# Performance work log

Measured on AMD Instinct MI355X. Metric: run time of the kernel, lower is better.

Reference implementation:

```python
import jax, jax.numpy as jnp
import numpy as np

EPS = 1e-5  # BatchNorm eps (torch default)

def setup_inputs() -> dict:
    key = jax.random.key(0)
    ks = jax.random.split(key, 24)
    B, NX, NY, F = 8, 128, 128, 128
    dims = [2 * F, 512, 256, 128, 64]
    d = {
        'x': jax.random.normal(ks[0], (B, NX, F), dtype=jnp.float32),
        'y': jax.random.normal(ks[1], (B, NY, F), dtype=jnp.float32),
    }
    i = 2
    for li, (din, dout) in enumerate(zip(dims[:-1], dims[1:]), start=1):
        d[f'w{li}'] = jax.random.normal(ks[i], (dout, din), dtype=jnp.float32) * (1.0 / np.sqrt(din)); i += 1
        d[f'b{li}'] = jax.random.normal(ks[i], (dout,), dtype=jnp.float32) * 0.02; i += 1
        if li < 4:  # BatchNorm1d on hidden layers only (eval mode: running stats)
            d[f'g{li}'] = 1.0 + 0.1 * jax.random.normal(ks[i], (dout,), dtype=jnp.float32); i += 1
            d[f'be{li}'] = 0.1 * jax.random.normal(ks[i], (dout,), dtype=jnp.float32); i += 1
            d[f'm{li}'] = 0.1 * jax.random.normal(ks[i], (dout,), dtype=jnp.float32); i += 1
            d[f'v{li}'] = 0.5 + jax.random.uniform(ks[i], (dout,), dtype=jnp.float32); i += 1
    return d

def _bn(h, g, be, m, v):
    # BatchNorm1d in eval mode over the channel (last) axis
    return (h - m) * (g * jax.lax.rsqrt(v + EPS)) + be

def reference(x, y,
              w1, b1, g1, be1, m1, v1,
              w2, b2, g2, be2, m2, v2,
              w3, b3, g3, be3, m3, v3,
              w4, b4):
    F = x.shape[-1]
    # First Linear on cat([x_i, y_j]) == split-weight broadcast add: avoids the
    # (B,nx,ny,2F) pairwise concat the torch code materializes (same math).
    wx, wy = w1[:, :F], w1[:, F:]                      # (512,F) each
    hx = jnp.einsum('bif,hf->bih', x, wx)              # (B,nx,512)
    hy = jnp.einsum('bjf,hf->bjh', y, wy)              # (B,ny,512)
    h = hx[:, :, None, :] + hy[:, None, :, :] + b1     # (B,nx,ny,512)
    h = jax.nn.relu(_bn(h, g1, be1, m1, v1))           # dropout is identity in eval
    h = jax.nn.relu(_bn(jnp.einsum('bijh,oh->bijo', h, w2) + b2, g2, be2, m2, v2))
    h = jax.nn.relu(_bn(jnp.einsum('bijh,oh->bijo', h, w3) + b3, g3, be3, m3, v3))
    e = jnp.einsum('bijh,oh->bijo', h, w4) + b4        # (B,nx,ny,64) embeddings
    # PSD path: einsum('bijk,bilk->bijl', e, e).sum(-1)
    #         == sum_k e[b,i,j,k] * (sum_l e[b,i,l,k])  -- avoids (B,nx,ny,ny)
    s = e.sum(axis=2)                                  # (B,nx,64)
    kernel = jnp.einsum('bijk,bik->bij', e, s)         # (B,nx,ny)
    return kernel
```

## Files before the change

### kernel.cpp

```cpp
#include <hip/hip_runtime.h>

#define EPS 1e-5f

typedef _Float16 half8 __attribute__((ext_vector_type(8)));
typedef _Float16 half4 __attribute__((ext_vector_type(4)));
typedef float f32x16 __attribute__((ext_vector_type(16)));
typedef float f32x4v __attribute__((ext_vector_type(4)));

__global__ __launch_bounds__(256)
void pre_kernel(
    const float* __restrict__ x, const float* __restrict__ y,
    const float* __restrict__ w1, const float* __restrict__ b1,
    const float* __restrict__ g1, const float* __restrict__ be1,
    const float* __restrict__ m1, const float* __restrict__ v1,
    const float* __restrict__ w2, const float* __restrict__ b2,
    const float* __restrict__ g2, const float* __restrict__ be2,
    const float* __restrict__ m2, const float* __restrict__ v2,
    const float* __restrict__ w3, const float* __restrict__ b3,
    const float* __restrict__ g3, const float* __restrict__ be3,
    const float* __restrict__ m3, const float* __restrict__ v3,
    const float* __restrict__ w4,
    _Float16* __restrict__ hxh, _Float16* __restrict__ hyh,
    _Float16* __restrict__ w2h, _Float16* __restrict__ w3h,
    _Float16* __restrict__ w4h,
    float* __restrict__ b2f, float* __restrict__ b3f)
{
    const int t = threadIdx.x;

    if (blockIdx.x >= 256) {
        int tid = (blockIdx.x - 256) * 256 + t;
        const int nth = 64 * 256;
        for (int idx = tid; idx < 256 * 512; idx += nth) {
            int n = idx >> 9;
            float a = g2[n] * rsqrtf(v2[n] + EPS);
            w2h[idx] = (_Float16)(a * w2[idx]);
        }
        for (int idx = tid; idx < 128 * 256; idx += nth) {
            int n = idx >> 8;
            float a = g3[n] * rsqrtf(v3[n] + EPS);
            w3h[idx] = (_Float16)(a * w3[idx]);
        }
        for (int idx = tid; idx < 64 * 128; idx += nth) {
            w4h[idx] = (_Float16)w4[idx];
        }
        if (tid < 256) {
            float a = g2[tid] * rsqrtf(v2[tid] + EPS);
            b2f[tid] = a * b2[tid] + be2[tid] - m2[tid] * a;
        } else if (tid < 384) {
            int n = tid - 256;
            float a = g3[n] * rsqrtf(v3[n] + EPS);
            b3f[n] = a * b3[n] + be3[n] - m3[n] * a;
        }
        return;
    }

    const int rg = blockIdx.x & 31;
    const int ng = (blockIdx.x >> 5) & 3;
    const int which = blockIdx.x >> 7;

    constexpr int LDA = 136;
    __shared__ _Float16 sh[32 * 136 + 128 * 136] __attribute__((aligned(16)));
    _Float16* xa = sh;
    _Float16* wb = sh + 32 * 136;

    const int rowbase = rg * 32;
    const float* src = which ? y : x;

#pragma unroll
    for (int p = 0; p < 4; ++p) {
        int c = p * 256 + t;
        int r = c >> 5, fo = (c & 31) * 4;
        f32x4v v = *(const f32x4v*)(src + (size_t)(rowbase + r) * 128 + fo);
        half4 h; h[0] = (_Float16)v[0]; h[1] = (_Float16)v[1];
        h[2] = (_Float16)v[2]; h[3] = (_Float16)v[3];
        *(half4*)(xa + r * LDA + fo) = h;
    }
#pragma unroll
    for (int p = 0; p < 16; ++p) {
        int c = p * 256 + t;
        int n = c >> 5, fo = (c & 31) * 4;
        f32x4v v = *(const f32x4v*)(w1 + (size_t)(ng * 128 + n) * 256 + which * 128 + fo);
        half4 h; h[0] = (_Float16)v[0]; h[1] = (_Float16)v[1];
        h[2] = (_Float16)v[2]; h[3] = (_Float16)v[3];
        *(half4*)(wb + n * LDA + fo) = h;
    }
    __syncthreads();

    const int wid = t >> 6;
    const int l = t & 63;
    const int l31 = l & 31, lh = l >> 5;

    f32x16 acc = (f32x16)0.f;
#pragma unroll
    for (int kc = 0; kc < 8; ++kc) {
        half8 af = *(const half8*)(xa + l31 * LDA + kc * 16 + lh * 8);
        half8 bf = *(const half8*)(wb + (wid * 32 + l31) * LDA + kc * 16 + lh * 8);
        acc = __builtin_amdgcn_mfma_f32_32x32x16_f16(af, bf, acc, 0, 0, 0);
    }

    const int n = ng * 128 + wid * 32 + l31;
    float alpha = g1[n] * rsqrtf(v1[n] + EPS);
    float bias = which ? 0.f : (alpha * b1[n] + be1[n] - m1[n] * alpha);
    _Float16* dst = which ? hyh : hxh;
#pragma unroll
    for (int r = 0; r < 16; ++r) {
        int m = (r & 3) + 8 * (r >> 2) + 4 * lh;
        dst[(size_t)(rowbase + m) * 512 + n] = (_Float16)(alpha * acc[r] + bias);
    }
}

__global__ __launch_bounds__(512, 4)
void fused_kernel(
    const _Float16* __restrict__ hxh, const _Float16* __restrict__ hyh,
    const _Float16* __restrict__ w2h, const _Float16* __restrict__ w3h,
    const _Float16* __restrict__ w4h,
    const float* __restrict__ b2f, const float* __restrict__ b3f,
    const float* __restrict__ b4,
    float* __restrict__ out)
{
    constexpr int LDK = 40;
    constexpr int LD2 = 264;
    constexpr int LD3 = 136;
    constexpr int LDE = 68;

    __shared__ char smem[3584 + 67584] __attribute__((aligned(16)));
    _Float16* hxs = (_Float16*)smem;
    float* spart  = (float*)(smem + 1024);
    float* ss     = (float*)(smem + 3072);
    char* R1 = smem + 3584;
    _Float16* a1t0 = (_Float16*)R1;
    _Float16* w2t0 = (_Float16*)(R1 + 10240);
    _Float16* a1t1 = (_Float16*)(R1 + 30720);
    _Float16* w2t1 = (_Float16*)(R1 + 40960);
    _Float16* a2  = (_Float16*)R1;
    _Float16* a3  = (_Float16*)R1;
    float*    es  = (float*)R1;

    const int b = blockIdx.x >> 7;
    const int i = blockIdx.x & 127;
    const int t = threadIdx.x;
    const int wid = t >> 6;
    const int l   = t & 63;
    const int l31 = l & 31;
    const int lh  = l >> 5;

    if (t < 64)
        *(half8*)(hxs + t * 8) = *(const half8*)(hxh + (size_t)(b * 128 + i) * 512 + t * 8);
    __syncthreads();

    const int wm = wid >> 2, wn = wid & 3;
    const size_t hyb = (size_t)b * 65536;

    f32x16 acc2[2][2];
#pragma unroll
    for (int mt = 0; mt < 2; ++mt)
#pragma unroll
        for (int nt = 0; nt < 2; ++nt) acc2[mt][nt] = (f32x16)0.f;

    const int sj = t >> 2, sq = t & 3;
    const int wn0 = t >> 2, wc0 = t & 3;
    const int wn1 = (t + 512) >> 2;

    half8 ra, rx, rw0, rw1;

    auto LOAD = [&](int kt) {
        const int k0 = kt * 32;
        ra  = *(const half8*)(hyh + hyb + (size_t)sj * 512 + k0 + sq * 8);
        rx  = *(const half8*)(hxs + k0 + sq * 8);
        rw0 = *(const half8*)(w2h + (size_t)wn0 * 512 + k0 + wc0 * 8);
        rw1 = *(const half8*)(w2h + (size_t)wn1 * 512 + k0 + wc0 * 8);
    };
    auto WRITE = [&](_Float16* A, _Float16* W) {
        half8 o;
#pragma unroll
        for (int c = 0; c < 8; ++c) {
            _Float16 v = (_Float16)(ra[c] + rx[c]);
            o[c] = v > (_Float16)0.f ? v : (_Float16)0.f;
        }
        *(half8*)(A + sj * LDK + sq * 8) = o;
        *(half8*)(W + wn0 * LDK + wc0 * 8) = rw0;
        *(half8*)(W + wn1 * LDK + wc0 * 8) = rw1;
    };
    auto MFMA2 = [&](const _Float16* A, const _Float16* W) {
#pragma unroll
        for (int kc = 0; kc < 2; ++kc) {
            half8 af0 = *(const half8*)(A + (wm * 64 + l31) * LDK + kc * 16 + lh * 8);
            half8 af1 = *(const half8*)(A + (wm * 64 + 32 + l31) * LDK + kc * 16 + lh * 8);
            half8 bf0 = *(const half8*)(W + (wn * 64 + l31) * LDK + kc * 16 + lh * 8);
            half8 bf1 = *(const half8*)(W + (wn * 64 + 32 + l31) * LDK + kc * 16 + lh * 8);
            acc2[0][0] = __builtin_amdgcn_mfma_f32_32x32x16_f16(af0, bf0, acc2[0][0], 0, 0, 0);
            acc2[1][0] = __builtin_amdgcn_mfma_f32_32x32x16_f16(af1, bf0, acc2[1][0], 0, 0, 0);
            acc2[0][1] = __builtin_amdgcn_mfma_f32_32x32x16_f16(af0, bf1, acc2[0][1], 0, 0, 0);
            acc2[1][1] = __builtin_amdgcn_mfma_f32_32x32x16_f16(af1, bf1, acc2[1][1], 0, 0, 0);
        }
    };

    LOAD(0);
    WRITE(a1t0, w2t0);
    __syncthreads();
#pragma unroll 2
    for (int kt = 0; kt < 16; ++kt) {
        const int cur = kt & 1;
        if (kt < 15) LOAD(kt + 1);
        MFMA2(cur ? a1t1 : a1t0, cur ? w2t1 : w2t0);
        if (kt < 15) WRITE(cur ? a1t0 : a1t1, cur ? w2t0 : w2t1);
        __syncthreads();
    }

    {
        float bb0 = b2f[wn * 64 + l31];
        float bb1 = b2f[wn * 64 + 32 + l31];
#pragma unroll
        for (int mt = 0; mt < 2; ++mt)
#pragma unroll
            for (int r = 0; r < 16; ++r) {
                int m = wm * 64 + mt * 32 + (r & 3) + 8 * (r >> 2) + 4 * lh;
                a2[m * LD2 + wn * 64 + l31]      = (_Float16)fmaxf(acc2[mt][0][r] + bb0, 0.f);
                a2[m * LD2 + wn * 64 + 32 + l31] = (_Float16)fmaxf(acc2[mt][1][r] + bb1, 0.f);
            }
    }
    __syncthreads();

    f32x16 acc3[2];
    acc3[0] = (f32x16)0.f; acc3[1] = (f32x16)0.f;
#pragma unroll 8
    for (int kc = 0; kc < 16; ++kc) {
        half8 bfr = *(const half8*)(w3h + (size_t)(wn * 32 + l31) * 256 + kc * 16 + lh * 8);
        half8 af0 = *(const half8*)(a2 + (wm * 64 + l31) * LD2 + kc * 16 + lh * 8);
        half8 af1 = *(const half8*)(a2 + (wm * 64 + 32 + l31) * LD2 + kc * 16 + lh * 8);
        acc3[0] = __builtin_amdgcn_mfma_f32_32x32x16_f16(af0, bfr, acc3[0], 0, 0, 0);
        acc3[1] = __builtin_amdgcn_mfma_f32_32x32x16_f16(af1, bfr, acc3[1], 0, 0, 0);
    }
    __syncthreads();
    {
        float b3v = b3f[wn * 32 + l31];
#pragma unroll
        for (int mt = 0; mt < 2; ++mt)
#pragma unroll
            for (int r = 0; r < 16; ++r) {
                int m = wm * 64 + mt * 32 + (r & 3) + 8 * (r >> 2) + 4 * lh;
                a3[m * LD3 + wn * 32 + l31] = (_Float16)fmaxf(acc3[mt][r] + b3v, 0.f);
            }
    }
    __syncthreads();

    const int wm4 = wid >> 1, wn4 = wid & 1;
    f32x16 acc4 = (f32x16)0.f;
#pragma unroll
    for (int kc = 0; kc < 8; ++kc) {
        half8 afr = *(const half8*)(a3 + (wm4 * 32 + l31) * LD3 + kc * 16 + lh * 8);
        half8 bfr = *(const half8*)(w4h + (size_t)(wn4 * 32 + l31) * 128 + kc * 16 + lh * 8);
        acc4 = __builtin_amdgcn_mfma_f32_32x32x16_f16(afr, bfr, acc4, 0, 0, 0);
    }
    __syncthreads();
    {
        float b4v = b4[wn4 * 32 + l31];
#pragma unroll
        for (int r = 0; r < 16; ++r) {
            int m = wm4 * 32 + (r & 3) + 8 * (r >> 2) + 4 * lh;
            es[m * LDE + wn4 * 32 + l31] = acc4[r] + b4v;
        }
    }
    __syncthreads();

    {
        float sv = 0.f;
#pragma unroll
        for (int jj = 0; jj < 16; ++jj) sv += es[(wid + jj * 8) * LDE + l];
        spart[wid * 64 + l] = sv;
    }
    __syncthreads();
    if (t < 64) {
        float s2 = 0.f;
#pragma unroll
        for (int r = 0; r < 8; ++r) s2 += spart[r * 64 + t];
        ss[t] = s2;
    }
    __syncthreads();
    {
        const int j = t >> 2, q = t & 3;
        float p = 0.f;
#pragma unroll
        for (int c = 0; c < 16; ++c) {
            int k = q + 4 * c;
            p += es[j * LDE + k] * ss[k];
        }
        p += __shfl_xor(p, 1);
        p += __shfl_xor(p, 2);
        if (q == 0) out[(size_t)(b * 128 + i) * 128 + j] = p;
    }
}

extern "C" void kernel_launch(void* const* d_in, const int* in_sizes, int n_in,
                              void* d_out, int out_size, void* d_ws, size_t ws_size,
                              hipStream_t stream)
{
    (void)in_sizes; (void)n_in; (void)out_size; (void)ws_size;

    const float* x   = (const float*)d_in[0];
    const float* y   = (const float*)d_in[1];
    const float* w1  = (const float*)d_in[2];
    const float* b1  = (const float*)d_in[3];
    const float* g1  = (const float*)d_in[4];
    const float* be1 = (const float*)d_in[5];
    const float* m1  = (const float*)d_in[6];
    const float* v1  = (const float*)d_in[7];
    const float* w2  = (const float*)d_in[8];
    const float* b2  = (const float*)d_in[9];
    const float* g2  = (const float*)d_in[10];
    const float* be2 = (const float*)d_in[11];
    const float* m2  = (const float*)d_in[12];
    const float* v2  = (const float*)d_in[13];
    const float* w3  = (const float*)d_in[14];
    const float* b3  = (const float*)d_in[15];
    const float* g3  = (const float*)d_in[16];
    const float* be3 = (const float*)d_in[17];
    const float* m3  = (const float*)d_in[18];
    const float* v3  = (const float*)d_in[19];
    const float* w4  = (const float*)d_in[20];
    const float* b4  = (const float*)d_in[21];
    float* out = (float*)d_out;

    float* b2f = (float*)d_ws;
    float* b3f = b2f + 256;
    _Float16* w2h = (_Float16*)(b3f + 128);
    _Float16* w3h = w2h + 131072;
    _Float16* w4h = w3h + 32768;
    _Float16* hxh = w4h + 8192;
    _Float16* hyh = hxh + 524288;

    hipLaunchKernelGGL(pre_kernel, dim3(320), dim3(256), 0, stream,
                       x, y, w1, b1, g1, be1, m1, v1,
                       w2, b2, g2, be2, m2, v2,
                       w3, b3, g3, be3, m3, v3,
                       w4,
                       hxh, hyh, w2h, w3h, w4h, b2f, b3f);

    hipLaunchKernelGGL(fused_kernel, dim3(1024), dim3(512), 0, stream,
                       hxh, hyh, w2h, w3h, w4h, b2f, b3f, b4, out);
}
```

Measured before the change: 73.86 us.

## Load layer-2 A fragments directly into registers and swizzle W2 LDS tiles

The layer-2 GEMM no longer stages the hx+hy ReLU activations through shared memory. Each wave loads its hy rows straight from global memory into MFMA fragment registers and applies the add and ReLU in registers. Only W2 tiles go through LDS, now unpadded with an XOR swizzle to avoid bank conflicts. Block indexing is also changed so consecutive blocks cover different batches, which alters L2 locality for hy and W2. The cost is more registers and redundant global loads of hy across the four waves that share the same rows.

```diff
diff --git a/kernel.cpp b/kernel.cpp
--- a/kernel.cpp
+++ b/kernel.cpp
@@ -118,7 +118,6 @@
     const float* __restrict__ b4,
     float* __restrict__ out)
 {
-    constexpr int LDK = 40;
     constexpr int LD2 = 264;
     constexpr int LD3 = 136;
     constexpr int LDE = 68;
@@ -128,16 +127,14 @@
     float* spart  = (float*)(smem + 1024);
     float* ss     = (float*)(smem + 3072);
     char* R1 = smem + 3584;
-    _Float16* a1t0 = (_Float16*)R1;
-    _Float16* w2t0 = (_Float16*)(R1 + 10240);
-    _Float16* a1t1 = (_Float16*)(R1 + 30720);
-    _Float16* w2t1 = (_Float16*)(R1 + 40960);
+    _Float16* w2t0 = (_Float16*)R1;
+    _Float16* w2t1 = (_Float16*)(R1 + 16384);
     _Float16* a2  = (_Float16*)R1;
     _Float16* a3  = (_Float16*)R1;
     float*    es  = (float*)R1;
 
-    const int b = blockIdx.x >> 7;
-    const int i = blockIdx.x & 127;
+    const int b = blockIdx.x & 7;
+    const int i = blockIdx.x >> 3;
     const int t = threadIdx.x;
     const int wid = t >> 6;
     const int l   = t & 63;
@@ -157,53 +154,72 @@
 #pragma unroll
         for (int nt = 0; nt < 2; ++nt) acc2[mt][nt] = (f32x16)0.f;
 
-    const int sj = t >> 2, sq = t & 3;
-    const int wn0 = t >> 2, wc0 = t & 3;
-    const int wn1 = (t + 512) >> 2;
-
-    half8 ra, rx, rw0, rw1;
-
-    auto LOAD = [&](int kt) {
-        const int k0 = kt * 32;
-        ra  = *(const half8*)(hyh + hyb + (size_t)sj * 512 + k0 + sq * 8);
-        rx  = *(const half8*)(hxs + k0 + sq * 8);
-        rw0 = *(const half8*)(w2h + (size_t)wn0 * 512 + k0 + wc0 * 8);
-        rw1 = *(const half8*)(w2h + (size_t)wn1 * 512 + k0 + wc0 * 8);
+    const int sn = t >> 1, kc2 = (t & 1) * 2;
+    const int fW = (sn >> 1) & 3;
+    const int fB = (l31 >> 1) & 3;
+
+    const _Float16* hyr0 = hyh + hyb + (size_t)(wm * 64 + l31) * 512 + lh * 8;
+    const _Float16* hyr1 = hyr0 + 32 * 512;
+
+    half8 rw0, rw1;
+    half8 raA[2][2], raB[2][2];
+
+    auto LOADW = [&](int kt) {
+        const _Float16* wp = w2h + (size_t)sn * 512 + kt * 32 + kc2 * 8;
+        rw0 = *(const half8*)wp;
+        rw1 = *(const half8*)(wp + 8);
     };
-    auto WRITE = [&](_Float16* A, _Float16* W) {
-        half8 o;
-#pragma unroll
-        for (int c = 0; c < 8; ++c) {
-            _Float16 v = (_Float16)(ra[c] + rx[c]);
-            o[c] = v > (_Float16)0.f ? v : (_Float16)0.f;
-        }
-        *(half8*)(A + sj * LDK + sq * 8) = o;
-        *(half8*)(W + wn0 * LDK + wc0 * 8) = rw0;
-        *(half8*)(W + wn1 * LDK + wc0 * 8) = rw1;
+    auto WRITEW = [&](_Float16* W) {
+        *(half8*)(W + sn * 32 + ((kc2 ^ fW) << 3))       = rw0;
+        *(half8*)(W + sn * 32 + (((kc2 + 1) ^ fW) << 3)) = rw1;
     };
-    auto MFMA2 = [&](const _Float16* A, const _Float16* W) {
-#pragma unroll
-        for (int kc = 0; kc < 2; ++kc) {
-            half8 af0 = *(const half8*)(A + (wm * 64 + l31) * LDK + kc * 16 + lh * 8);
-            half8 af1 = *(const half8*)(A + (wm * 64 + 32 + l31) * LDK + kc * 16 + lh * 8);
-            half8 bf0 = *(const half8*)(W + (wn * 64 + l31) * LDK + kc * 16 + lh * 8);
-            half8 bf1 = *(const half8*)(W + (wn * 64 + 32 + l31) * LDK + kc * 16 + lh * 8);
-            acc2[0][0] = __builtin_amdgcn_mfma_f32_32x32x16_f16(af0, bf0, acc2[0][0], 0, 0, 0);
-            acc2[1][0] = __builtin_amdgcn_mfma_f32_32x32x16_f16(af1, bf0, acc2[1][0], 0, 0, 0);
-            acc2[0][1] = __builtin_amdgcn_mfma_f32_32x32x16_f16(af0, bf1, acc2[0][1], 0, 0, 0);
-            acc2[1][1] = __builtin_amdgcn_mfma_f32_32x32x16_f16(af1, bf1, acc2[1][1], 0, 0, 0);
+    auto LOADA = [&](half8 (&ra)[2][2], int kt) {
+#pragma unroll
+        for (int kk = 0; kk < 2; ++kk) {
+            ra[kk][0] = *(const half8*)(hyr0 + kt * 32 + kk * 16);
+            ra[kk][1] = *(const half8*)(hyr1 + kt * 32 + kk * 16);
         }
     };
-
-    LOAD(0);
-    WRITE(a1t0, w2t0);
-    __syncthreads();
-#pragma unroll 2
-    for (int kt = 0; kt < 16; ++kt) {
-        const int cur = kt & 1;
-        if (kt < 15) LOAD(kt + 1);
-        MFMA2(cur ? a1t1 : a1t0, cur ? w2t1 : w2t0);
-        if (kt < 15) WRITE(cur ? a1t0 : a1t1, cur ? w2t0 : w2t1);
+    auto MFMASTEP = [&](const _Float16* W, half8 (&ra)[2][2], int kt) {
+#pragma unroll
+        for (int kk = 0; kk < 2; ++kk) {
+            half8 rx = *(const half8*)(hxs + kt * 32 + kk * 16 + lh * 8);
+            half8 af[2], bf[2];
+#pragma unroll
+            for (int mt = 0; mt < 2; ++mt) {
+                half8 s = ra[kk][mt] + rx;
+#pragma unroll
+                for (int c = 0; c < 8; ++c)
+                    af[mt][c] = s[c] > (_Float16)0.f ? s[c] : (_Float16)0.f;
+            }
+#pragma unroll
+            for (int nt = 0; nt < 2; ++nt)
+                bf[nt] = *(const half8*)(W + (wn * 64 + nt * 32 + l31) * 32 +
+                                         (((kk * 2 + lh) ^ fB) << 3));
+            acc2[0][0] = __builtin_amdgcn_mfma_f32_32x32x16_f16(af[0], bf[0], acc2[0][0], 0, 0, 0);
+            acc2[1][0] = __builtin_amdgcn_mfma_f32_32x32x16_f16(af[1], bf[0], acc2[1][0], 0, 0, 0);
+            acc2[0][1] = __builtin_amdgcn_mfma_f32_32x32x16_f16(af[0], bf[1], acc2[0][1], 0, 0, 0);
+            acc2[1][1] = __builtin_amdgcn_mfma_f32_32x32x16_f16(af[1], bf[1], acc2[1][1], 0, 0, 0);
+        }
+    };
+
+    LOADA(raA, 0);
+    LOADW(0);
+    WRITEW(w2t0);
+    __syncthreads();
+
+    for (int kt = 0; kt < 16; kt += 2) {
+        LOADW(kt + 1);
+        LOADA(raB, kt + 1);
+        MFMASTEP(w2t0, raA, kt);
+        WRITEW(w2t1);
+        __syncthreads();
+        if (kt + 2 < 16) {
+            LOADW(kt + 2);
+            LOADA(raA, kt + 2);
+        }
+        MFMASTEP(w2t1, raB, kt + 1);
+        if (kt + 2 < 16) WRITEW(w2t0);
         __syncthreads();
     }
 
```

New measurement: 113.4 us. 53.5% more time.

## Pre-swizzle weights and hy into MFMA fragment layout, load layer-2 operands directly

Applied to the files above, without the earlier changes.

The pre-kernel now writes w2/w3/w4 and hy in a fragment-major layout where each 32x16 MFMA operand tile is contiguous, so every lane reads one coalesced half8. The layer-2 GEMM in the fused kernel drops its LDS double-buffered staging and barriers and instead loads A and B fragments straight from global memory into registers, software-pipelined two k-steps deep. The hx add and ReLU are applied in registers. Each wave now fetches its own operands from global/L2 instead of sharing them through LDS, which raises redundant global traffic across waves.

```diff
diff --git a/kernel.cpp b/kernel.cpp
--- a/kernel.cpp
+++ b/kernel.cpp
@@ -6,6 +6,7 @@
 typedef _Float16 half4 __attribute__((ext_vector_type(4)));
 typedef float f32x16 __attribute__((ext_vector_type(16)));
 typedef float f32x4v __attribute__((ext_vector_type(4)));
+
 
 __global__ __launch_bounds__(256)
 void pre_kernel(
@@ -31,17 +32,21 @@
         int tid = (blockIdx.x - 256) * 256 + t;
         const int nth = 64 * 256;
         for (int idx = tid; idx < 256 * 512; idx += nth) {
-            int n = idx >> 9;
+            int n = idx >> 9, k = idx & 511;
             float a = g2[n] * rsqrtf(v2[n] + EPS);
-            w2h[idx] = (_Float16)(a * w2[idx]);
+            int addr = ((n >> 5) * 32 + (k >> 4)) * 512 + ((k >> 3) & 1) * 256 + (n & 31) * 8 + (k & 7);
+            w2h[addr] = (_Float16)(a * w2[idx]);
         }
         for (int idx = tid; idx < 128 * 256; idx += nth) {
-            int n = idx >> 8;
+            int n = idx >> 8, k = idx & 255;
             float a = g3[n] * rsqrtf(v3[n] + EPS);
-            w3h[idx] = (_Float16)(a * w3[idx]);
+            int addr = ((n >> 5) * 16 + (k >> 4)) * 512 + ((k >> 3) & 1) * 256 + (n & 31) * 8 + (k & 7);
+            w3h[addr] = (_Float16)(a * w3[idx]);
         }
         for (int idx = tid; idx < 64 * 128; idx += nth) {
-            w4h[idx] = (_Float16)w4[idx];
+            int n = idx >> 7, k = idx & 127;
+            int addr = ((n >> 5) * 8 + (k >> 4)) * 512 + ((k >> 3) & 1) * 256 + (n & 31) * 8 + (k & 7);
+            w4h[addr] = (_Float16)w4[idx];
         }
         if (tid < 256) {
             float a = g2[tid] * rsqrtf(v2[tid] + EPS);
@@ -100,12 +105,23 @@
 
     const int n = ng * 128 + wid * 32 + l31;
     float alpha = g1[n] * rsqrtf(v1[n] + EPS);
-    float bias = which ? 0.f : (alpha * b1[n] + be1[n] - m1[n] * alpha);
-    _Float16* dst = which ? hyh : hxh;
-#pragma unroll
-    for (int r = 0; r < 16; ++r) {
-        int m = (r & 3) + 8 * (r >> 2) + 4 * lh;
-        dst[(size_t)(rowbase + m) * 512 + n] = (_Float16)(alpha * acc[r] + bias);
+    if (which == 0) {
+        float bias = alpha * b1[n] + be1[n] - m1[n] * alpha;
+#pragma unroll
+        for (int r = 0; r < 16; ++r) {
+            int m = (r & 3) + 8 * (r >> 2) + 4 * lh;
+            hxh[(size_t)(rowbase + m) * 512 + n] = (_Float16)(alpha * acc[r] + bias);
+        }
+    } else {
+        const int ks = n >> 4, lhh = (n >> 3) & 1, c = n & 7;
+#pragma unroll
+        for (int r = 0; r < 16; ++r) {
+            int m = (r & 3) + 8 * (r >> 2) + 4 * lh;
+            int R = rowbase + m;
+            int bb = R >> 7, j = R & 127;
+            int addr = bb * 65536 + ((j >> 5) * 32 + ks) * 512 + lhh * 256 + (j & 31) * 8 + c;
+            hyh[addr] = (_Float16)(alpha * acc[r]);
+        }
     }
 }
 
@@ -118,7 +134,6 @@
     const float* __restrict__ b4,
     float* __restrict__ out)
 {
-    constexpr int LDK = 40;
     constexpr int LD2 = 264;
     constexpr int LD3 = 136;
     constexpr int LDE = 68;
@@ -128,10 +143,6 @@
     float* spart  = (float*)(smem + 1024);
     float* ss     = (float*)(smem + 3072);
     char* R1 = smem + 3584;
-    _Float16* a1t0 = (_Float16*)R1;
-    _Float16* w2t0 = (_Float16*)(R1 + 10240);
-    _Float16* a1t1 = (_Float16*)(R1 + 30720);
-    _Float16* w2t1 = (_Float16*)(R1 + 40960);
     _Float16* a2  = (_Float16*)R1;
     _Float16* a3  = (_Float16*)R1;
     float*    es  = (float*)R1;
@@ -149,7 +160,6 @@
     __syncthreads();
 
     const int wm = wid >> 2, wn = wid & 3;
-    const size_t hyb = (size_t)b * 65536;
 
     f32x16 acc2[2][2];
 #pragma unroll
@@ -157,54 +167,43 @@
 #pragma unroll
         for (int nt = 0; nt < 2; ++nt) acc2[mt][nt] = (f32x16)0.f;
 
-    const int sj = t >> 2, sq = t & 3;
-    const int wn0 = t >> 2, wc0 = t & 3;
-    const int wn1 = (t + 512) >> 2;
-
-    half8 ra, rx, rw0, rw1;
-
-    auto LOAD = [&](int kt) {
-        const int k0 = kt * 32;
-        ra  = *(const half8*)(hyh + hyb + (size_t)sj * 512 + k0 + sq * 8);
-        rx  = *(const half8*)(hxs + k0 + sq * 8);
-        rw0 = *(const half8*)(w2h + (size_t)wn0 * 512 + k0 + wc0 * 8);
-        rw1 = *(const half8*)(w2h + (size_t)wn1 * 512 + k0 + wc0 * 8);
+    const _Float16* paf0 = hyh + (size_t)b * 65536 + (wm * 2) * 32 * 512 + l * 8;
+    const _Float16* paf1 = paf0 + 32 * 512;
+    const _Float16* pbf0 = w2h + (wn * 2) * 32 * 512 + l * 8;
+    const _Float16* pbf1 = pbf0 + 32 * 512;
+
+    auto LD = [&](half8& A0, half8& A1, half8& B0, half8& B1, int ks) {
+        A0 = *(const half8*)(paf0 + ks * 512);
+        A1 = *(const half8*)(paf1 + ks * 512);
+        B0 = *(const half8*)(pbf0 + ks * 512);
+        B1 = *(const half8*)(pbf1 + ks * 512);
     };
-    auto WRITE = [&](_Float16* A, _Float16* W) {
-        half8 o;
+    auto STEP = [&](half8 A0, half8 A1, half8 B0, half8 B1, int ks) {
+        half8 rx = *(const half8*)(hxs + ks * 16 + lh * 8);
+        half8 s0 = A0 + rx;
+        half8 s1 = A1 + rx;
+        half8 af0, af1;
 #pragma unroll
         for (int c = 0; c < 8; ++c) {
-            _Float16 v = (_Float16)(ra[c] + rx[c]);
-            o[c] = v > (_Float16)0.f ? v : (_Float16)0.f;
-        }
-        *(half8*)(A + sj * LDK + sq * 8) = o;
-        *(half8*)(W + wn0 * LDK + wc0 * 8) = rw0;
-        *(half8*)(W + wn1 * LDK + wc0 * 8) = rw1;
+            af0[c] = s0[c] > (_Float16)0.f ? s0[c] : (_Float16)0.f;
+            af1[c] = s1[c] > (_Float16)0.f ? s1[c] : (_Float16)0.f;
+        }
+        acc2[0][0] = __builtin_amdgcn_mfma_f32_32x32x16_f16(af0, B0, acc2[0][0], 0, 0, 0);
+        acc2[1][0] = __builtin_amdgcn_mfma_f32_32x32x16_f16(af1, B0, acc2[1][0], 0, 0, 0);
+        acc2[0][1] = __builtin_amdgcn_mfma_f32_32x32x16_f16(af0, B1, acc2[0][1], 0, 0, 0);
+        acc2[1][1] = __builtin_amdgcn_mfma_f32_32x32x16_f16(af1, B1, acc2[1][1], 0, 0, 0);
     };
-    auto MFMA2 = [&](const _Float16* A, const _Float16* W) {
-#pragma unroll
-        for (int kc = 0; kc < 2; ++kc) {
-            half8 af0 = *(const half8*)(A + (wm * 64 + l31) * LDK + kc * 16 + lh * 8);
-            half8 af1 = *(const half8*)(A + (wm * 64 + 32 + l31) * LDK + kc * 16 + lh * 8);
-            half8 bf0 = *(const half8*)(W + (wn * 64 + l31) * LDK + kc * 16 + lh * 8);
-            half8 bf1 = *(const half8*)(W + (wn * 64 + 32 + l31) * LDK + kc * 16 + lh * 8);
-            acc2[0][0] = __builtin_amdgcn_mfma_f32_32x32x16_f16(af0, bf0, acc2[0][0], 0, 0, 0);
-            acc2[1][0] = __builtin_amdgcn_mfma_f32_32x32x16_f16(af1, bf0, acc2[1][0], 0, 0, 0);
-            acc2[0][1] = __builtin_amdgcn_mfma_f32_32x32x16_f16(af0, bf1, acc2[0][1], 0, 0, 0);
-            acc2[1][1] = __builtin_amdgcn_mfma_f32_32x32x16_f16(af1, bf1, acc2[1][1], 0, 0, 0);
-        }
-    };
-
-    LOAD(0);
-    WRITE(a1t0, w2t0);
-    __syncthreads();
+
+    {
+        half8 cA0, cA1, cB0, cB1, nA0, nA1, nB0, nB1;
+        LD(cA0, cA1, cB0, cB1, 0);
 #pragma unroll 2
-    for (int kt = 0; kt < 16; ++kt) {
-        const int cur = kt & 1;
-        if (kt < 15) LOAD(kt + 1);
-        MFMA2(cur ? a1t1 : a1t0, cur ? w2t1 : w2t0);
-        if (kt < 15) WRITE(cur ? a1t0 : a1t1, cur ? w2t0 : w2t1);
-        __syncthreads();
+        for (int ks = 0; ks < 32; ks += 2) {
+            LD(nA0, nA1, nB0, nB1, ks + 1);
+            STEP(cA0, cA1, cB0, cB1, ks);
+            if (ks + 2 < 32) LD(cA0, cA1, cB0, cB1, ks + 2);
+            STEP(nA0, nA1, nB0, nB1, ks + 1);
+        }
     }
 
     {
@@ -225,7 +224,7 @@
     acc3[0] = (f32x16)0.f; acc3[1] = (f32x16)0.f;
 #pragma unroll 8
     for (int kc = 0; kc < 16; ++kc) {
-        half8 bfr = *(const half8*)(w3h + (size_t)(wn * 32 + l31) * 256 + kc * 16 + lh * 8);
+        half8 bfr = *(const half8*)(w3h + (wn * 16 + kc) * 512 + l * 8);
         half8 af0 = *(const half8*)(a2 + (wm * 64 + l31) * LD2 + kc * 16 + lh * 8);
         half8 af1 = *(const half8*)(a2 + (wm * 64 + 32 + l31) * LD2 + kc * 16 + lh * 8);
         acc3[0] = __builtin_amdgcn_mfma_f32_32x32x16_f16(af0, bfr, acc3[0], 0, 0, 0);
@@ -249,7 +248,7 @@
 #pragma unroll
     for (int kc = 0; kc < 8; ++kc) {
         half8 afr = *(const half8*)(a3 + (wm4 * 32 + l31) * LD3 + kc * 16 + lh * 8);
-        half8 bfr = *(const half8*)(w4h + (size_t)(wn4 * 32 + l31) * 128 + kc * 16 + lh * 8);
+        half8 bfr = *(const half8*)(w4h + (wn4 * 8 + kc) * 512 + l * 8);
         acc4 = __builtin_amdgcn_mfma_f32_32x32x16_f16(afr, bfr, acc4, 0, 0, 0);
     }
     __syncthreads();
```

New measurement: 67.42 us. 1.1x faster.
